# Kernel optimization log

Hardware: AMD Instinct MI355X
Metric: run time of the kernel (lower is better)

## Reference

```python
import jax, jax.numpy as jnp
import numpy as np

B, L, H = 1, 2048, 2048          # batch, seq_len, hidden_size
E, N, K, R = 4096, 16, 4, 128    # intermediate, ssm_state, conv_kernel, dt_rank


def setup_inputs() -> dict:
    key = jax.random.key(0)
    ks = jax.random.split(key, 8)
    s = 0.02
    inp = {
        "hidden_states": jax.random.normal(ks[0], (B, L, H), jnp.float32),
        "in_proj_w": jax.random.normal(ks[1], (2 * E, H), jnp.float32) * s,
        "conv_w": jax.random.normal(ks[2], (E, 1, K), jnp.float32) * s,
        "conv_b": jax.random.normal(ks[3], (E,), jnp.float32) * s,
        "x_proj_w": jax.random.normal(ks[4], (R + 2 * N, E), jnp.float32) * s,
        "dt_proj_w": jax.random.normal(ks[5], (E, R), jnp.float32) * s,
        "dt_proj_b": jax.random.normal(ks[6], (E,), jnp.float32) * s,
        "A_log": jnp.broadcast_to(jnp.log(jnp.arange(1, N + 1, dtype=jnp.float32))[None, :], (E, N)).copy(),
        "D": jnp.ones((E,), jnp.float32),
        "out_proj_w": jax.random.normal(ks[7], (H, E), jnp.float32) * s,
    }
    return inp


def _mamba_mixer(hidden_states, in_proj_w, conv_w, conv_b, x_proj_w,
                 dt_proj_w, dt_proj_b, A_log, D, out_proj_w):
    # in_proj -> [B, L, 2E], split into hidden / gate
    proj = jnp.einsum('blh,eh->ble', hidden_states, in_proj_w)
    h, gate = jnp.split(proj, 2, axis=-1)            # each [B, L, E]

    # depthwise causal conv1d over time, padding K-1 on the left
    h_c = h.transpose(0, 2, 1)                       # [B, E, L]
    h_c = jax.lax.conv_general_dilated(
        h_c, conv_w, window_strides=(1,), padding=[(K - 1, 0)],
        feature_group_count=E, dimension_numbers=('NCH', 'OIH', 'NCH'))
    h_c = h_c + conv_b[None, :, None]
    h = jax.nn.silu(h_c).transpose(0, 2, 1)          # [B, L, E]

    # x_proj -> dt, B, C (input-dependent SSM params)
    ssm = jnp.einsum('ble,pe->blp', h, x_proj_w)     # [B, L, R+2N]
    dt, Bp, Cp = jnp.split(ssm, [R, R + N], axis=-1)
    dt = jax.nn.softplus(jnp.einsum('blr,er->ble', dt, dt_proj_w) + dt_proj_b)  # [B,L,E]

    A = -jnp.exp(A_log)                              # [E, N]
    dA = jnp.exp(dt[..., None] * A)                  # [B, L, E, N]
    dBu = (dt * h)[..., None] * Bp[:, :, None, :]    # [B, L, E, N]

    # selective scan: s_t = dA_t * s_{t-1} + dBu_t
    def step(s, xs):
        dA_t, dBu_t = xs
        s = s * dA_t + dBu_t
        return s, s

    s0 = jnp.zeros((h.shape[0], E, N), h.dtype)
    _, states = jax.lax.scan(step, s0, (dA.transpose(1, 0, 2, 3), dBu.transpose(1, 0, 2, 3)))
    # states: [L, B, E, N]
    y = jnp.einsum('lben,bln->ble', states, Cp)      # [B, L, E]
    y = y + h * D                                    # skip via D
    y = y * jax.nn.silu(gate)                        # gated output
    return jnp.einsum('ble,he->blh', y, out_proj_w)  # [B, L, H]


def reference(hidden_states, in_proj_w, conv_w, conv_b, x_proj_w,
              dt_proj_w, dt_proj_b, A_log, D, out_proj_w):
    return _mamba_mixer(hidden_states, in_proj_w, conv_w, conv_b, x_proj_w,
                        dt_proj_w, dt_proj_b, A_log, D, out_proj_w)
```

## Files before the change

### kernel.cpp

```cpp
#include <hip/hip_runtime.h>

#define LL 2048
#define HH 2048
#define EE 4096
#define NS 16
#define RR 128
#define CT 32
#define NC (LL / CT)
#define BM 128
#define BN 128
#define BK 64

typedef __bf16 bf16x8 __attribute__((ext_vector_type(8)));
typedef float f32x4 __attribute__((ext_vector_type(4)));

__device__ __forceinline__ unsigned short f2bf(float f) {
  union { float f; unsigned int u; } v; v.f = f;
  unsigned int r = v.u + 0x7fffu + ((v.u >> 16) & 1u);
  return (unsigned short)(r >> 16);
}

__device__ __forceinline__ float bf2f(unsigned short u) {
  union { unsigned int i; float f; } v;
  v.i = ((unsigned int)u) << 16;
  return v.f;
}

__device__ __forceinline__ float softplus_fast(float x) {
  if (x > 20.0f) return x;
  float e = __builtin_amdgcn_exp2f(1.44269504f * x);
  return 0.69314718f * __builtin_amdgcn_logf(1.0f + e);
}

__device__ __forceinline__ void async_cp16(const unsigned short* g,
                                           unsigned short* l) {
  __builtin_amdgcn_global_load_lds(
      (const __attribute__((address_space(1))) unsigned int*)g,
      (__attribute__((address_space(3))) unsigned int*)l, 16, 0, 0);
}

__global__ void cast_bf16_k(const float* __restrict__ in,
                            unsigned short* __restrict__ out, int n4) {
  int i = blockIdx.x * blockDim.x + threadIdx.x;
  if (i >= n4) return;
  float4 v = reinterpret_cast<const float4*>(in)[i];
  ushort4 o;
  o.x = f2bf(v.x); o.y = f2bf(v.y); o.z = f2bf(v.z); o.w = f2bf(v.w);
  reinterpret_cast<ushort4*>(out)[i] = o;
}

__global__ void zero_k(float* __restrict__ p, int n4) {
  int i = blockIdx.x * blockDim.x + threadIdx.x;
  if (i >= n4) return;
  float4 z; z.x = z.y = z.z = z.w = 0.0f;
  reinterpret_cast<float4*>(p)[i] = z;
}

template <int EPI>
__global__ __launch_bounds__(512, 2) void gemm256(
    const unsigned short* __restrict__ A,
    const unsigned short* __restrict__ B,
    float* __restrict__ C,
    int M, int N, int K, int tilesM, int splitk,
    float* __restrict__ auxF, unsigned short* __restrict__ auxB) {
  __shared__ __align__(16) unsigned short As[2][16384];
  __shared__ __align__(16) unsigned short Bs[2][16384];

  int bid = blockIdx.x;
  int tnInner = bid & 7;
  int rest = bid >> 3;
  int tm = rest % tilesM;
  int tn = (rest / tilesM) * 8 + tnInner;

  int Kslice = K / splitk;
  int k_begin = blockIdx.y * Kslice;
  int NT = Kslice / 64;

  int tid = threadIdx.x;
  int lane = tid & 63;
  int wave = tid >> 6;
  int wm = wave >> 2;
  int wn = wave & 3;
  int m16 = lane & 15, quad = lane >> 4;

  const unsigned short* Ab = A + (size_t)tm * 256 * K;
  const unsigned short* Bb = B + (size_t)tn * 256 * K;

  int rowS = tid >> 3;
  int gcbS = (tid & 7) ^ (rowS & 7);
  int ldsWB = (tid & ~63) * 8;

  int sw = m16 & 7;
  int coff0 = (quad ^ sw) << 3;
  int coff1 = ((4 + quad) ^ sw) << 3;
  int aoff = (wm * 128 + m16) * 64;
  int boff = (wn * 64 + m16) * 64;

  f32x4 acc[8][4];
#pragma unroll
  for (int i = 0; i < 8; ++i)
#pragma unroll
    for (int j = 0; j < 4; ++j)
#pragma unroll
      for (int t = 0; t < 4; ++t) acc[i][j][t] = 0.0f;

#pragma unroll
  for (int c = 0; c < 4; ++c)
    async_cp16(Ab + (size_t)(c * 64 + rowS) * K + k_begin + gcbS * 8,
               &As[0][c * 4096 + ldsWB]);
#pragma unroll
  for (int c = 0; c < 4; ++c)
    async_cp16(Bb + (size_t)(c * 64 + rowS) * K + k_begin + gcbS * 8,
               &Bs[0][c * 4096 + ldsWB]);
  if (NT > 1) {
    async_cp16(Ab + (size_t)(rowS)*K + k_begin + 64 + gcbS * 8,
               &As[1][0 * 4096 + ldsWB]);
    async_cp16(Ab + (size_t)(64 + rowS) * K + k_begin + 64 + gcbS * 8,
               &As[1][1 * 4096 + ldsWB]);
    asm volatile("s_waitcnt vmcnt(2)" ::: "memory");
  } else {
    asm volatile("s_waitcnt vmcnt(0)" ::: "memory");
  }
  __builtin_amdgcn_s_barrier();

  auto tile_body = [&](int t, int buf) {
    unsigned short* Acur = &As[buf][0];
    unsigned short* Bcur = &Bs[buf][0];
    unsigned short* Anxt = &As[buf ^ 1][0];
    unsigned short* Bnxt = &Bs[buf ^ 1][0];
    int ktn = k_begin + (t + 1) * 64;
    int ktn2 = k_begin + (t + 2) * 64;
    bool h1 = (t + 1 < NT), h2 = (t + 2 < NT);
    bf16x8 a[4][2], b[2][2];

#pragma unroll
    for (int i = 0; i < 4; ++i) {
      a[i][0] = *reinterpret_cast<const bf16x8*>(&Acur[aoff + i * 1024 + coff0]);
      a[i][1] = *reinterpret_cast<const bf16x8*>(&Acur[aoff + i * 1024 + coff1]);
    }
#pragma unroll
    for (int j = 0; j < 2; ++j) {
      b[j][0] = *reinterpret_cast<const bf16x8*>(&Bcur[boff + j * 1024 + coff0]);
      b[j][1] = *reinterpret_cast<const bf16x8*>(&Bcur[boff + j * 1024 + coff1]);
    }
    if (h1) {
      async_cp16(Ab + (size_t)(128 + rowS) * K + ktn + gcbS * 8,
                 Anxt + 2 * 4096 + ldsWB);
      async_cp16(Ab + (size_t)(192 + rowS) * K + ktn + gcbS * 8,
                 Anxt + 3 * 4096 + ldsWB);
    }
    __builtin_amdgcn_s_barrier();
    asm volatile("s_waitcnt lgkmcnt(0)" ::: "memory");
    __builtin_amdgcn_sched_barrier(0);
    __builtin_amdgcn_s_setprio(1);
#pragma unroll
    for (int i = 0; i < 4; ++i)
#pragma unroll
      for (int j = 0; j < 2; ++j) {
        acc[i][j] = __builtin_amdgcn_mfma_f32_16x16x32_bf16(a[i][0], b[j][0], acc[i][j], 0, 0, 0);
        acc[i][j] = __builtin_amdgcn_mfma_f32_16x16x32_bf16(a[i][1], b[j][1], acc[i][j], 0, 0, 0);
      }
    __builtin_amdgcn_s_setprio(0);
    __builtin_amdgcn_s_barrier();

#pragma unroll
    for (int j = 0; j < 2; ++j) {
      b[j][0] = *reinterpret_cast<const bf16x8*>(&Bcur[boff + (2 + j) * 1024 + coff0]);
      b[j][1] = *reinterpret_cast<const bf16x8*>(&Bcur[boff + (2 + j) * 1024 + coff1]);
    }
    if (h1) {
      async_cp16(Bb + (size_t)(rowS)*K + ktn + gcbS * 8, Bnxt + 0 * 4096 + ldsWB);
      async_cp16(Bb + (size_t)(64 + rowS) * K + ktn + gcbS * 8,
                 Bnxt + 1 * 4096 + ldsWB);
    }
    __builtin_amdgcn_s_barrier();
    asm volatile("s_waitcnt lgkmcnt(0)" ::: "memory");
    __builtin_amdgcn_sched_barrier(0);
    __builtin_amdgcn_s_setprio(1);
#pragma unroll
    for (int i = 0; i < 4; ++i)
#pragma unroll
      for (int j = 0; j < 2; ++j) {
        acc[i][2 + j] = __builtin_amdgcn_mfma_f32_16x16x32_bf16(a[i][0], b[j][0], acc[i][2 + j], 0, 0, 0);
        acc[i][2 + j] = __builtin_amdgcn_mfma_f32_16x16x32_bf16(a[i][1], b[j][1], acc[i][2 + j], 0, 0, 0);
      }
    __builtin_amdgcn_s_setprio(0);
    __builtin_amdgcn_s_barrier();

#pragma unroll
    for (int i = 0; i < 4; ++i) {
      a[i][0] = *reinterpret_cast<const bf16x8*>(&Acur[aoff + (4 + i) * 1024 + coff0]);
      a[i][1] = *reinterpret_cast<const bf16x8*>(&Acur[aoff + (4 + i) * 1024 + coff1]);
    }
    if (h1) {
      async_cp16(Bb + (size_t)(128 + rowS) * K + ktn + gcbS * 8,
                 Bnxt + 2 * 4096 + ldsWB);
      async_cp16(Bb + (size_t)(192 + rowS) * K + ktn + gcbS * 8,
                 Bnxt + 3 * 4096 + ldsWB);
    }
    __builtin_amdgcn_s_barrier();
    asm volatile("s_waitcnt lgkmcnt(0)" ::: "memory");
    __builtin_amdgcn_sched_barrier(0);
    __builtin_amdgcn_s_setprio(1);
#pragma unroll
    for (int i = 0; i < 4; ++i)
#pragma unroll
      for (int j = 0; j < 2; ++j) {
        acc[4 + i][2 + j] = __builtin_amdgcn_mfma_f32_16x16x32_bf16(a[i][0], b[j][0], acc[4 + i][2 + j], 0, 0, 0);
        acc[4 + i][2 + j] = __builtin_amdgcn_mfma_f32_16x16x32_bf16(a[i][1], b[j][1], acc[4 + i][2 + j], 0, 0, 0);
      }
    __builtin_amdgcn_s_setprio(0);
    __builtin_amdgcn_s_barrier();

#pragma unroll
    for (int j = 0; j < 2; ++j) {
      b[j][0] = *reinterpret_cast<const bf16x8*>(&Bcur[boff + j * 1024 + coff0]);
      b[j][1] = *reinterpret_cast<const bf16x8*>(&Bcur[boff + j * 1024 + coff1]);
    }
    asm volatile("s_waitcnt lgkmcnt(0)" ::: "memory");
    __builtin_amdgcn_sched_barrier(0);
    __builtin_amdgcn_s_barrier();
    if (h2) {
      async_cp16(Ab + (size_t)(rowS)*K + ktn2 + gcbS * 8,
                 Acur + 0 * 4096 + ldsWB);
      async_cp16(Ab + (size_t)(64 + rowS) * K + ktn2 + gcbS * 8,
                 Acur + 1 * 4096 + ldsWB);
    }
    __builtin_amdgcn_s_setprio(1);
#pragma unroll
    for (int i = 0; i < 4; ++i)
#pragma unroll
      for (int j = 0; j < 2; ++j) {
        acc[4 + i][j] = __builtin_amdgcn_mfma_f32_16x16x32_bf16(a[i][0], b[j][0], acc[4 + i][j], 0, 0, 0);
        acc[4 + i][j] = __builtin_amdgcn_mfma_f32_16x16x32_bf16(a[i][1], b[j][1], acc[4 + i][j], 0, 0, 0);
      }
    __builtin_amdgcn_s_setprio(0);
    if (h2) {
      asm volatile("s_waitcnt vmcnt(2)" ::: "memory");
    } else {
      asm volatile("s_waitcnt vmcnt(0)" ::: "memory");
    }
    __builtin_amdgcn_s_barrier();
  };

  for (int t = 0; t < NT; t += 2) {
    tile_body(t, 0);
    tile_body(t + 1, 1);
  }

  int rowB = tm * 256 + wm * 128;
  int colB = tn * 256 + wn * 64;
  if constexpr (EPI == 1) {
#pragma unroll
    for (int mi = 0; mi < 8; ++mi)
#pragma unroll
      for (int nj = 0; nj < 4; ++nj) {
        int col = colB + nj * 16 + m16;
        int row0 = rowB + mi * 16 + quad * 4;
#pragma unroll
        for (int t4 = 0; t4 < 4; ++t4)
          atomicAdd(&C[(size_t)(row0 + t4) * N + col], acc[mi][nj][t4]);
      }
  } else {
    if (colB < EE) {
#pragma unroll
      for (int mi = 0; mi < 8; ++mi)
#pragma unroll
        for (int nj = 0; nj < 4; ++nj) {
          int col = colB + nj * 16 + m16;
          int row0 = rowB + mi * 16 + quad * 4;
#pragma unroll
          for (int t4 = 0; t4 < 4; ++t4)
            auxF[(size_t)(row0 + t4) * EE + col] = acc[mi][nj][t4];
        }
    } else {
#pragma unroll
      for (int mi = 0; mi < 8; ++mi)
#pragma unroll
        for (int nj = 0; nj < 4; ++nj) {
          int cg = colB + nj * 16 + m16 - EE;
          int row0 = rowB + mi * 16 + quad * 4;
#pragma unroll
          for (int t4 = 0; t4 < 4; ++t4) {
            float v = acc[mi][nj][t4];
            float s = v / (1.0f + __expf(-v));
            auxB[(size_t)(row0 + t4) * EE + cg] = f2bf(s);
          }
        }
    }
  }
}

template <int EPI>
__global__ __launch_bounds__(256) void gemm_lds_t(
    const unsigned short* __restrict__ A,
    const unsigned short* __restrict__ B,
    float* __restrict__ C,
    int M, int N, int K, int tilesM, int splitk,
    const float* __restrict__ bias, float* __restrict__ auxF,
    unsigned short* __restrict__ auxB) {
  __shared__ __align__(16) unsigned short As[BM * BK];
  __shared__ __align__(16) unsigned short Bs[BN * BK];

  int bid = blockIdx.x;
  int tnInner = bid & 7;
  int rest = bid >> 3;
  int tm = rest % tilesM;
  int tnOuter = rest / tilesM;
  int tn = tnOuter * 8 + tnInner;

  int Kslice = K / splitk;
  int k_begin = blockIdx.y * Kslice;
  int k_end = k_begin + Kslice;

  int tid = threadIdx.x;
  int lane = tid & 63;
  int wave = tid >> 6;
  int wm = wave & 1, wn = wave >> 1;
  int m16 = lane & 15, quad = lane >> 4;

  const unsigned short* Ab = A + (size_t)tm * BM * K;
  const unsigned short* Bb = B + (size_t)tn * BN * K;

  int srow[4], sgcb[4];
#pragma unroll
  for (int it = 0; it < 4; ++it) {
    int blk = it * 256 + tid;
    srow[it] = blk >> 3;
    sgcb[it] = (blk & 7) ^ (srow[it] & 7);
  }
  int ldsbase = (tid & ~63) * 8;

  f32x4 acc[4][4];
#pragma unroll
  for (int i = 0; i < 4; ++i)
#pragma unroll
    for (int j = 0; j < 4; ++j)
#pragma unroll
      for (int t = 0; t < 4; ++t) acc[i][j][t] = 0.0f;

  for (int k0 = k_begin; k0 < k_end; k0 += BK) {
    __syncthreads();
#pragma unroll
    for (int it = 0; it < 4; ++it)
      async_cp16(Ab + (size_t)srow[it] * K + k0 + sgcb[it] * 8,
                 &As[it * 2048 + ldsbase]);
#pragma unroll
    for (int it = 0; it < 4; ++it)
      async_cp16(Bb + (size_t)srow[it] * K + k0 + sgcb[it] * 8,
                 &Bs[it * 2048 + ldsbase]);
    __syncthreads();
#pragma unroll
    for (int kk = 0; kk < 2; ++kk) {
      bf16x8 a[4], b[4];
#pragma unroll
      for (int i = 0; i < 4; ++i) {
        int rr = wm * 64 + i * 16 + m16;
        int cb = (kk << 2) + quad;
        a[i] = *reinterpret_cast<const bf16x8*>(
            &As[rr * BK + ((cb ^ (rr & 7)) << 3)]);
      }
#pragma unroll
      for (int j = 0; j < 4; ++j) {
        int rr = wn * 64 + j * 16 + m16;
        int cb = (kk << 2) + quad;
        b[j] = *reinterpret_cast<const bf16x8*>(
            &Bs[rr * BK + ((cb ^ (rr & 7)) << 3)]);
      }
#pragma unroll
      for (int i = 0; i < 4; ++i)
#pragma unroll
        for (int j = 0; j < 4; ++j)
          acc[i][j] =
              __builtin_amdgcn_mfma_f32_16x16x32_bf16(a[i], b[j], acc[i][j], 0, 0, 0);
    }
  }

  int rowB = tm * BM + wm * 64;
  int colB = tn * BN + wn * 64;
  if constexpr (EPI == 1) {
#pragma unroll
    for (int i = 0; i < 4; ++i)
#pragma unroll
      for (int j = 0; j < 4; ++j) {
        int col = colB + j * 16 + m16;
        int row0 = rowB + i * 16 + quad * 4;
#pragma unroll
        for (int t = 0; t < 4; ++t)
          atomicAdd(&C[(size_t)(row0 + t) * N + col], acc[i][j][t]);
      }
  } else {
#pragma unroll
    for (int i = 0; i < 4; ++i)
#pragma unroll
      for (int j = 0; j < 4; ++j) {
        int col = colB + j * 16 + m16;
        float bv = bias[col];
        int row0 = rowB + i * 16 + quad * 4;
#pragma unroll
        for (int t = 0; t < 4; ++t) {
          float x = acc[i][j][t] + bv;
          auxB[(size_t)(row0 + t) * EE + col] = f2bf(softplus_fast(x));
        }
      }
  }
}

__global__ __launch_bounds__(256) void gemm_bt(
    const unsigned short* __restrict__ A,
    const unsigned short* __restrict__ B,
    float* __restrict__ C,
    int M, int N, int K, int tilesN, int splitk) {
  int bid = blockIdx.x;
  int groupSize = 8 * tilesN;
  int g = bid / groupSize, r = bid % groupSize;
  int tm = g * 8 + (r & 7);
  int tn = r >> 3;

  int Kslice = K / splitk;
  int k_begin = blockIdx.y * Kslice;
  int k_end = k_begin + Kslice;

  int tid = threadIdx.x;
  int wave = tid >> 6, lane = tid & 63;
  int wm = wave & 1, wn = wave >> 1;
  int m16 = lane & 15, quad = lane >> 4;
  int rowBase = tm * 64 + wm * 32;
  int colBase = tn * 128 + wn * 64;

  const unsigned short* a0p = A + (size_t)(rowBase + m16) * K + quad * 8;
  const unsigned short* a1p = A + (size_t)(rowBase + 16 + m16) * K + quad * 8;
  const unsigned short* bp[4];
  bool bok[4];
#pragma unroll
  for (int j = 0; j < 4; ++j) {
    int col = colBase + j * 16 + m16;
    bok[j] = (col < N);
    bp[j] = B + (size_t)(bok[j] ? col : 0) * K + quad * 8;
  }

  f32x4 acc[2][4];
#pragma unroll
  for (int i = 0; i < 2; ++i)
#pragma unroll
    for (int j = 0; j < 4; ++j)
#pragma unroll
      for (int t = 0; t < 4; ++t) acc[i][j][t] = 0.0f;

  bf16x8 zero8;
#pragma unroll
  for (int t = 0; t < 8; ++t) zero8[t] = (__bf16)0.0f;

  for (int k = k_begin; k < k_end; k += 32) {
    bf16x8 a0 = *reinterpret_cast<const bf16x8*>(a0p + k);
    bf16x8 a1 = *reinterpret_cast<const bf16x8*>(a1p + k);
    bf16x8 b[4];
#pragma unroll
    for (int j = 0; j < 4; ++j)
      b[j] = bok[j] ? *reinterpret_cast<const bf16x8*>(bp[j] + k) : zero8;
#pragma unroll
    for (int j = 0; j < 4; ++j) {
      acc[0][j] = __builtin_amdgcn_mfma_f32_16x16x32_bf16(a0, b[j], acc[0][j], 0, 0, 0);
      acc[1][j] = __builtin_amdgcn_mfma_f32_16x16x32_bf16(a1, b[j], acc[1][j], 0, 0, 0);
    }
  }

#pragma unroll
  for (int i = 0; i < 2; ++i)
#pragma unroll
    for (int j = 0; j < 4; ++j) {
      int col = colBase + j * 16 + m16;
      if (col >= N) continue;
      int row0 = rowBase + i * 16 + quad * 4;
      if (splitk == 1) {
#pragma unroll
        for (int t = 0; t < 4; ++t)
          C[(size_t)(row0 + t) * N + col] = acc[i][j][t];
      } else {
#pragma unroll
        for (int t = 0; t < 4; ++t)
          atomicAdd(&C[(size_t)(row0 + t) * N + col], acc[i][j][t]);
      }
    }
}

__global__ __launch_bounds__(256) void conv_silu_k(
    const float* __restrict__ projh, const float* __restrict__ cw,
    const float* __restrict__ cb, unsigned short* __restrict__ hb) {
  int e = blockIdx.x * 256 + threadIdx.x;
  int l0 = blockIdx.y * 16;
  float w0 = cw[e * 4 + 0], w1 = cw[e * 4 + 1];
  float w2 = cw[e * 4 + 2], w3 = cw[e * 4 + 3];
  float bias = cb[e];
  float xm3 = (l0 >= 3) ? projh[(size_t)(l0 - 3) * EE + e] : 0.0f;
  float xm2 = (l0 >= 2) ? projh[(size_t)(l0 - 2) * EE + e] : 0.0f;
  float xm1 = (l0 >= 1) ? projh[(size_t)(l0 - 1) * EE + e] : 0.0f;
#pragma unroll
  for (int t = 0; t < 16; ++t) {
    int l = l0 + t;
    float x0 = projh[(size_t)l * EE + e];
    float acc = bias + w0 * xm3 + w1 * xm2 + w2 * xm1 + w3 * x0;
    float s = acc / (1.0f + __expf(-acc));
    hb[(size_t)l * EE + e] = f2bf(s);
    xm3 = xm2; xm2 = xm1; xm1 = x0;
  }
}

__global__ void dtcast_k(const float* __restrict__ ssm,
                         unsigned short* __restrict__ dtin, int n) {
  int i = blockIdx.x * blockDim.x + threadIdx.x;
  if (i >= n) return;
  int l = i >> 7, r = i & 127;
  dtin[i] = f2bf(ssm[l * 160 + r]);
}

__global__ __launch_bounds__(256) void scan_partA(
    const unsigned short* __restrict__ dtb, const unsigned short* __restrict__ hb,
    const float* __restrict__ ssm, const float* __restrict__ A_log,
    float* __restrict__ P, float* __restrict__ S) {
  int e = blockIdx.y * 256 + threadIdx.x;
  int c = blockIdx.x;
  float Aa[16];
#pragma unroll
  for (int q = 0; q < 4; ++q) {
    float4 a = reinterpret_cast<const float4*>(&A_log[(size_t)e * NS])[q];
    Aa[q * 4 + 0] = -__expf(a.x) * 1.44269504f;
    Aa[q * 4 + 1] = -__expf(a.y) * 1.44269504f;
    Aa[q * 4 + 2] = -__expf(a.z) * 1.44269504f;
    Aa[q * 4 + 3] = -__expf(a.w) * 1.44269504f;
  }
  float s[16], p[16];
#pragma unroll
  for (int n = 0; n < 16; ++n) { s[n] = 0.0f; p[n] = 1.0f; }
  int l0 = c * CT;
#pragma unroll 2
  for (int t = 0; t < CT; ++t) {
    int l = l0 + t;
    size_t o = (size_t)l * EE + e;
    float dtv = bf2f(dtb[o]);
    float hv = bf2f(hb[o]);
    float Bv[16];
#pragma unroll
    for (int q = 0; q < 4; ++q)
      *reinterpret_cast<float4*>(&Bv[q * 4]) =
          reinterpret_cast<const float4*>(&ssm[(size_t)l * 160 + 128])[q];
    float z = dtv * hv;
#pragma unroll
    for (int n = 0; n < 16; ++n) {
      float dA = __builtin_amdgcn_exp2f(dtv * Aa[n]);
      s[n] = s[n] * dA + z * Bv[n];
      p[n] *= dA;
    }
  }
  size_t base = ((size_t)c * EE + e) * NS;
#pragma unroll
  for (int q = 0; q < 4; ++q) {
    reinterpret_cast<float4*>(&P[base])[q] = *reinterpret_cast<float4*>(&p[q * 4]);
    reinterpret_cast<float4*>(&S[base])[q] = *reinterpret_cast<float4*>(&s[q * 4]);
  }
}

__global__ __launch_bounds__(256) void scan_chunkB(
    const float* __restrict__ P, float* __restrict__ S) {
  int gidx = blockIdx.x * 256 + threadIdx.x;
  float s = 0.0f;
  float pv = P[gidx], sv = S[gidx];
  for (int c = 0; c < NC; ++c) {
    float pn = 0.0f, sn = 0.0f;
    if (c + 1 < NC) {
      size_t i2 = (size_t)(c + 1) * (EE * NS) + gidx;
      pn = P[i2];
      sn = S[i2];
    }
    float s_next = s * pv + sv;
    S[(size_t)c * (EE * NS) + gidx] = s;
    s = s_next;
    pv = pn; sv = sn;
  }
}

__global__ __launch_bounds__(256) void scan_partC(
    const unsigned short* __restrict__ dtb, const unsigned short* __restrict__ hb,
    const float* __restrict__ ssm, const float* __restrict__ A_log,
    const float* __restrict__ Dp, const unsigned short* __restrict__ sg,
    const float* __restrict__ Sinit, unsigned short* __restrict__ yb) {
  int e = blockIdx.y * 256 + threadIdx.x;
  int c = blockIdx.x;
  float Aa[16];
#pragma unroll
  for (int q = 0; q < 4; ++q) {
    float4 a = reinterpret_cast<const float4*>(&A_log[(size_t)e * NS])[q];
    Aa[q * 4 + 0] = -__expf(a.x) * 1.44269504f;
    Aa[q * 4 + 1] = -__expf(a.y) * 1.44269504f;
    Aa[q * 4 + 2] = -__expf(a.z) * 1.44269504f;
    Aa[q * 4 + 3] = -__expf(a.w) * 1.44269504f;
  }
  float Dv = Dp[e];
  float s[16];
  size_t base = ((size_t)c * EE + e) * NS;
#pragma unroll
  for (int q = 0; q < 4; ++q)
    *reinterpret_cast<float4*>(&s[q * 4]) =
        reinterpret_cast<const float4*>(&Sinit[base])[q];
  int l0 = c * CT;
#pragma unroll 2
  for (int t = 0; t < CT; ++t) {
    int l = l0 + t;
    size_t o = (size_t)l * EE + e;
    float dtv = bf2f(dtb[o]);
    float hv = bf2f(hb[o]);
    float Bv[16], Cv[16];
#pragma unroll
    for (int q = 0; q < 4; ++q) {
      *reinterpret_cast<float4*>(&Bv[q * 4]) =
          reinterpret_cast<const float4*>(&ssm[(size_t)l * 160 + 128])[q];
      *reinterpret_cast<float4*>(&Cv[q * 4]) =
          reinterpret_cast<const float4*>(&ssm[(size_t)l * 160 + 144])[q];
    }
    float z = dtv * hv;
    float y = 0.0f;
#pragma unroll
    for (int n = 0; n < 16; ++n) {
      float dA = __builtin_amdgcn_exp2f(dtv * Aa[n]);
      s[n] = s[n] * dA + z * Bv[n];
      y += s[n] * Cv[n];
    }
    float gv = bf2f(sg[o]);
    float yv = (y + hv * Dv) * gv;
    yb[o] = f2bf(yv);
  }
}

extern "C" void kernel_launch(void* const* d_in, const int* in_sizes, int n_in,
                              void* d_out, int out_size, void* d_ws, size_t ws_size,
                              hipStream_t stream) {
  const float* hs   = (const float*)d_in[0];
  const float* w1   = (const float*)d_in[1];
  const float* cw   = (const float*)d_in[2];
  const float* cb   = (const float*)d_in[3];
  const float* xw   = (const float*)d_in[4];
  const float* dtw  = (const float*)d_in[5];
  const float* dtb  = (const float*)d_in[6];
  const float* Alog = (const float*)d_in[7];
  const float* Dp   = (const float*)d_in[8];
  const float* ow   = (const float*)d_in[9];
  float* out = (float*)d_out;

  char* ws = (char*)d_ws;
  size_t off = 0;
  auto alloc = [&](size_t b) {
    char* p = ws + off;
    off += (b + 255) & ~(size_t)255;
    return p;
  };
  float* projh = (float*)alloc((size_t)LL * EE * 4);
  unsigned short* sg  = (unsigned short*)alloc((size_t)LL * EE * 2);
  unsigned short* hb  = (unsigned short*)alloc((size_t)LL * EE * 2);
  unsigned short* dtb_buf = (unsigned short*)alloc((size_t)LL * EE * 2);
  unsigned short* w1b = (unsigned short*)alloc((size_t)2 * EE * HH * 2);
  unsigned short* hsb = (unsigned short*)alloc((size_t)LL * HH * 2);
  unsigned short* yb  = (unsigned short*)alloc((size_t)LL * EE * 2);
  unsigned short* owb = (unsigned short*)alloc((size_t)HH * EE * 2);
  unsigned short* xwb = (unsigned short*)alloc((size_t)160 * EE * 2);
  float* ssm = (float*)alloc((size_t)LL * 160 * 4);
  unsigned short* dtin = (unsigned short*)alloc((size_t)LL * RR * 2);
  unsigned short* dtwb = (unsigned short*)alloc((size_t)EE * RR * 2);
  float* Pbuf = (float*)alloc((size_t)NC * EE * NS * 4);
  float* Sbuf = (float*)alloc((size_t)NC * EE * NS * 4);

  auto cast = [&](const float* in, unsigned short* o, int nelem) {
    int n4 = nelem / 4;
    cast_bf16_k<<<(n4 + 255) / 256, 256, 0, stream>>>(in, o, n4);
  };
  cast(hs, hsb, LL * HH);
  cast(w1, w1b, 2 * EE * HH);
  cast(xw, xwb, 160 * EE);
  cast(dtw, dtwb, EE * RR);
  cast(ow, owb, HH * EE);
  zero_k<<<(LL * 160 / 4 + 255) / 256, 256, 0, stream>>>(ssm, LL * 160 / 4);
  zero_k<<<(LL * HH / 4 + 255) / 256, 256, 0, stream>>>(out, LL * HH / 4);

  {
    int tilesM = LL / 256;
    int tilesN = (2 * EE) / 256;
    gemm256<2><<<dim3(tilesM * tilesN, 1), 512, 0, stream>>>(
        hsb, w1b, nullptr, LL, 2 * EE, HH, tilesM, 1, projh, sg);
  }
  conv_silu_k<<<dim3(EE / 256, LL / 16), 256, 0, stream>>>(projh, cw, cb, hb);
  {
    int tilesN = (160 + 127) / 128, tilesM = LL / 64;
    gemm_bt<<<dim3(tilesM * tilesN, 8), 256, 0, stream>>>(
        hb, xwb, ssm, LL, 160, EE, tilesN, 8);
  }
  dtcast_k<<<(LL * RR + 255) / 256, 256, 0, stream>>>(ssm, dtin, LL * RR);
  {
    int tilesN = EE / BN, tilesM = LL / BM;
    gemm_lds_t<4><<<dim3(tilesM * tilesN, 1), 256, 0, stream>>>(
        dtin, dtwb, nullptr, LL, EE, RR, tilesM, 1, dtb, nullptr, dtb_buf);
  }
  scan_partA<<<dim3(NC, EE / 256), 256, 0, stream>>>(dtb_buf, hb, ssm, Alog,
                                                     Pbuf, Sbuf);
  scan_chunkB<<<EE * NS / 256, 256, 0, stream>>>(Pbuf, Sbuf);
  scan_partC<<<dim3(NC, EE / 256), 256, 0, stream>>>(dtb_buf, hb, ssm, Alog, Dp,
                                                     sg, Sbuf, yb);
  {
    int tilesM = LL / 256, tilesN = HH / 256;
    gemm256<1><<<dim3(tilesM * tilesN, 4), 512, 0, stream>>>(
        yb, owb, out, LL, HH, EE, tilesM, 4, nullptr, nullptr);
  }
}
```

Measured before the change: 457.7 us.

## Simplify GEMM double-buffer: issue full next-tile prefetch upfront, keep B fragments in registers

```diff
diff --git a/kernel.cpp b/kernel.cpp
--- a/kernel.cpp
+++ b/kernel.cpp
@@ -112,26 +112,27 @@
   for (int c = 0; c < 4; ++c)
     async_cp16(Bb + (size_t)(c * 64 + rowS) * K + k_begin + gcbS * 8,
                &Bs[0][c * 4096 + ldsWB]);
-  if (NT > 1) {
-    async_cp16(Ab + (size_t)(rowS)*K + k_begin + 64 + gcbS * 8,
-               &As[1][0 * 4096 + ldsWB]);
-    async_cp16(Ab + (size_t)(64 + rowS) * K + k_begin + 64 + gcbS * 8,
-               &As[1][1 * 4096 + ldsWB]);
-    asm volatile("s_waitcnt vmcnt(2)" ::: "memory");
-  } else {
-    asm volatile("s_waitcnt vmcnt(0)" ::: "memory");
-  }
+  asm volatile("s_waitcnt vmcnt(0)" ::: "memory");
   __builtin_amdgcn_s_barrier();
 
   auto tile_body = [&](int t, int buf) {
     unsigned short* Acur = &As[buf][0];
     unsigned short* Bcur = &Bs[buf][0];
-    unsigned short* Anxt = &As[buf ^ 1][0];
-    unsigned short* Bnxt = &Bs[buf ^ 1][0];
-    int ktn = k_begin + (t + 1) * 64;
-    int ktn2 = k_begin + (t + 2) * 64;
-    bool h1 = (t + 1 < NT), h2 = (t + 2 < NT);
-    bf16x8 a[4][2], b[2][2];
+    if (t + 1 < NT) {
+      unsigned short* An = &As[buf ^ 1][0];
+      unsigned short* Bn = &Bs[buf ^ 1][0];
+      int kt = k_begin + (t + 1) * 64;
+#pragma unroll
+      for (int c = 0; c < 4; ++c)
+        async_cp16(Ab + (size_t)(c * 64 + rowS) * K + kt + gcbS * 8,
+                   An + c * 4096 + ldsWB);
+#pragma unroll
+      for (int c = 0; c < 4; ++c)
+        async_cp16(Bb + (size_t)(c * 64 + rowS) * K + kt + gcbS * 8,
+                   Bn + c * 4096 + ldsWB);
+    }
+
+    bf16x8 a[4][2], b0[2][2], b1[2][2];
 
 #pragma unroll
     for (int i = 0; i < 4; ++i) {
@@ -140,14 +141,8 @@
     }
 #pragma unroll
     for (int j = 0; j < 2; ++j) {
-      b[j][0] = *reinterpret_cast<const bf16x8*>(&Bcur[boff + j * 1024 + coff0]);
-      b[j][1] = *reinterpret_cast<const bf16x8*>(&Bcur[boff + j * 1024 + coff1]);
-    }
-    if (h1) {
-      async_cp16(Ab + (size_t)(128 + rowS) * K + ktn + gcbS * 8,
-                 Anxt + 2 * 4096 + ldsWB);
-      async_cp16(Ab + (size_t)(192 + rowS) * K + ktn + gcbS * 8,
-                 Anxt + 3 * 4096 + ldsWB);
+      b0[j][0] = *reinterpret_cast<const bf16x8*>(&Bcur[boff + j * 1024 + coff0]);
+      b0[j][1] = *reinterpret_cast<const bf16x8*>(&Bcur[boff + j * 1024 + coff1]);
     }
     __builtin_amdgcn_s_barrier();
     asm volatile("s_waitcnt lgkmcnt(0)" ::: "memory");
@@ -157,21 +152,16 @@
     for (int i = 0; i < 4; ++i)
 #pragma unroll
       for (int j = 0; j < 2; ++j) {
-        acc[i][j] = __builtin_amdgcn_mfma_f32_16x16x32_bf16(a[i][0], b[j][0], acc[i][j], 0, 0, 0);
-        acc[i][j] = __builtin_amdgcn_mfma_f32_16x16x32_bf16(a[i][1], b[j][1], acc[i][j], 0, 0, 0);
+        acc[i][j] = __builtin_amdgcn_mfma_f32_16x16x32_bf16(a[i][0], b0[j][0], acc[i][j], 0, 0, 0);
+        acc[i][j] = __builtin_amdgcn_mfma_f32_16x16x32_bf16(a[i][1], b0[j][1], acc[i][j], 0, 0, 0);
       }
     __builtin_amdgcn_s_setprio(0);
     __builtin_amdgcn_s_barrier();
 
 #pragma unroll
     for (int j = 0; j < 2; ++j) {
-      b[j][0] = *reinterpret_cast<const bf16x8*>(&Bcur[boff + (2 + j) * 1024 + coff0]);
-      b[j][1] = *reinterpret_cast<const bf16x8*>(&Bcur[boff + (2 + j) * 1024 + coff1]);
-    }
-    if (h1) {
-      async_cp16(Bb + (size_t)(rowS)*K + ktn + gcbS * 8, Bnxt + 0 * 4096 + ldsWB);
-      async_cp16(Bb + (size_t)(64 + rowS) * K + ktn + gcbS * 8,
-                 Bnxt + 1 * 4096 + ldsWB);
+      b1[j][0] = *reinterpret_cast<const bf16x8*>(&Bcur[boff + (2 + j) * 1024 + coff0]);
+      b1[j][1] = *reinterpret_cast<const bf16x8*>(&Bcur[boff + (2 + j) * 1024 + coff1]);
     }
     __builtin_amdgcn_s_barrier();
     asm volatile("s_waitcnt lgkmcnt(0)" ::: "memory");
@@ -181,8 +171,8 @@
     for (int i = 0; i < 4; ++i)
 #pragma unroll
       for (int j = 0; j < 2; ++j) {
-        acc[i][2 + j] = __builtin_amdgcn_mfma_f32_16x16x32_bf16(a[i][0], b[j][0], acc[i][2 + j], 0, 0, 0);
-        acc[i][2 + j] = __builtin_amdgcn_mfma_f32_16x16x32_bf16(a[i][1], b[j][1], acc[i][2 + j], 0, 0, 0);
+        acc[i][2 + j] = __builtin_amdgcn_mfma_f32_16x16x32_bf16(a[i][0], b1[j][0], acc[i][2 + j], 0, 0, 0);
+        acc[i][2 + j] = __builtin_amdgcn_mfma_f32_16x16x32_bf16(a[i][1], b1[j][1], acc[i][2 + j], 0, 0, 0);
       }
     __builtin_amdgcn_s_setprio(0);
     __builtin_amdgcn_s_barrier();
@@ -191,12 +181,6 @@
     for (int i = 0; i < 4; ++i) {
       a[i][0] = *reinterpret_cast<const bf16x8*>(&Acur[aoff + (4 + i) * 1024 + coff0]);
       a[i][1] = *reinterpret_cast<const bf16x8*>(&Acur[aoff + (4 + i) * 1024 + coff1]);
-    }
-    if (h1) {
-      async_cp16(Bb + (size_t)(128 + rowS) * K + ktn + gcbS * 8,
-                 Bnxt + 2 * 4096 + ldsWB);
-      async_cp16(Bb + (size_t)(192 + rowS) * K + ktn + gcbS * 8,
-                 Bnxt + 3 * 4096 + ldsWB);
     }
     __builtin_amdgcn_s_barrier();
     asm volatile("s_waitcnt lgkmcnt(0)" ::: "memory");
@@ -206,40 +190,22 @@
     for (int i = 0; i < 4; ++i)
 #pragma unroll
       for (int j = 0; j < 2; ++j) {
-        acc[4 + i][2 + j] = __builtin_amdgcn_mfma_f32_16x16x32_bf16(a[i][0], b[j][0], acc[4 + i][2 + j], 0, 0, 0);
-        acc[4 + i][2 + j] = __builtin_amdgcn_mfma_f32_16x16x32_bf16(a[i][1], b[j][1], acc[4 + i][2 + j], 0, 0, 0);
+        acc[4 + i][2 + j] = __builtin_amdgcn_mfma_f32_16x16x32_bf16(a[i][0], b1[j][0], acc[4 + i][2 + j], 0, 0, 0);
+        acc[4 + i][2 + j] = __builtin_amdgcn_mfma_f32_16x16x32_bf16(a[i][1], b1[j][1], acc[4 + i][2 + j], 0, 0, 0);
       }
     __builtin_amdgcn_s_setprio(0);
     __builtin_amdgcn_s_barrier();
 
-#pragma unroll
-    for (int j = 0; j < 2; ++j) {
-      b[j][0] = *reinterpret_cast<const bf16x8*>(&Bcur[boff + j * 1024 + coff0]);
-      b[j][1] = *reinterpret_cast<const bf16x8*>(&Bcur[boff + j * 1024 + coff1]);
-    }
-    asm volatile("s_waitcnt lgkmcnt(0)" ::: "memory");
-    __builtin_amdgcn_sched_barrier(0);
-    __builtin_amdgcn_s_barrier();
-    if (h2) {
-      async_cp16(Ab + (size_t)(rowS)*K + ktn2 + gcbS * 8,
-                 Acur + 0 * 4096 + ldsWB);
-      async_cp16(Ab + (size_t)(64 + rowS) * K + ktn2 + gcbS * 8,
-                 Acur + 1 * 4096 + ldsWB);
-    }
     __builtin_amdgcn_s_setprio(1);
 #pragma unroll
     for (int i = 0; i < 4; ++i)
 #pragma unroll
       for (int j = 0; j < 2; ++j) {
-        acc[4 + i][j] = __builtin_amdgcn_mfma_f32_16x16x32_bf16(a[i][0], b[j][0], acc[4 + i][j], 0, 0, 0);
-        acc[4 + i][j] = __builtin_amdgcn_mfma_f32_16x16x32_bf16(a[i][1], b[j][1], acc[4 + i][j], 0, 0, 0);
+        acc[4 + i][j] = __builtin_amdgcn_mfma_f32_16x16x32_bf16(a[i][0], b0[j][0], acc[4 + i][j], 0, 0, 0);
+        acc[4 + i][j] = __builtin_amdgcn_mfma_f32_16x16x32_bf16(a[i][1], b0[j][1], acc[4 + i][j], 0, 0, 0);
       }
     __builtin_amdgcn_s_setprio(0);
-    if (h2) {
-      asm volatile("s_waitcnt vmcnt(2)" ::: "memory");
-    } else {
-      asm volatile("s_waitcnt vmcnt(0)" ::: "memory");
-    }
+    asm volatile("s_waitcnt vmcnt(0)" ::: "memory");
     __builtin_amdgcn_s_barrier();
   };
 
```

Result: slower. 469.4 us (+2.6%).
